# Optimization experiments

Measured on AMD Instinct MI355X. Metric: run time of the kernel, lower is better.

Reference implementation:

```python
import jax, jax.numpy as jnp
import numpy as np

N, D, H2, E = 4096, 1024, 4096, 8  # tokens, input_dim, 2*hidden_dim, num_experts
H = H2 // 2


def setup_inputs() -> dict:
    key = jax.random.key(0)
    k1, k2, k3 = jax.random.split(key, 3)
    x = jax.random.normal(k1, (N, D), dtype=jnp.float32)
    expert_weights = jax.random.normal(k2, (E, D, H2), dtype=jnp.float32) * (1.0 / np.sqrt(D))
    expert_indices = jax.random.randint(k3, (N,), 0, E, dtype=jnp.int32)
    return {"x": x, "expert_weights": expert_weights, "expert_indices": expert_indices}


def reference(x, expert_weights, expert_indices):
    # Grouped GEMM equivalent: each token n is processed by expert e = expert_indices[n]:
    #   h_n = x_n @ W_e            -> [2H]
    #   out_n = silu(h[:H]) * h[H:] (SwiGLU)
    # jit-friendly dense-dispatch: project with all experts, then gather the assigned one.
    h_all = jnp.einsum('nd,edh->neh', x, expert_weights)            # [N, E, 2H]
    h = jnp.take_along_axis(h_all, expert_indices[:, None, None].astype(jnp.int32), axis=1)[:, 0]  # [N, 2H]
    a, b = h[:, :H], h[:, H:]
    return jax.nn.silu(a) * b                                        # [N, H]
```

## Files before the change

kernel.cpp:

```cpp
#include <hip/hip_runtime.h>
#include <hip/hip_bf16.h>

#define N_TOK 4096
#define DIM   1024
#define H2V   4096
#define HV    2048
#define NE    8
#define BM    128
#define BN    64
#define BK    64
#define NTHR  256
#define ROW_TILES (N_TOK / BM)

typedef __attribute__((ext_vector_type(4))) float  f32x4;
typedef __attribute__((ext_vector_type(2))) float  f32x2;
typedef __attribute__((ext_vector_type(8))) short  s16x8;

__device__ __forceinline__ unsigned short f2bf(float f) {
    __hip_bfloat16 h = __float2bfloat16(f);
    union { __hip_bfloat16 h; unsigned short u; } v;
    v.h = h;
    return v.u;
}

__global__ void k_init(int* __restrict__ counts) {
    if (threadIdx.x < NE) counts[threadIdx.x] = 0;
}

__global__ void k_scatter(const int* __restrict__ idx, int* __restrict__ counts,
                          unsigned short* __restrict__ slots) {
    int n = blockIdx.x * blockDim.x + threadIdx.x;
    if (n < N_TOK) {
        int e = idx[n];
        int p = atomicAdd(&counts[e], 1);
        slots[e * N_TOK + p] = (unsigned short)n;
    }
}

__global__ __launch_bounds__(NTHR, 2) void k_gemm(
        const float* __restrict__ X, const float* __restrict__ W,
        const int* __restrict__ counts, const unsigned short* __restrict__ slots,
        float* __restrict__ out) {
    const int ct = blockIdx.x;
    const int e  = blockIdx.y >> 5;
    const int rt = blockIdx.y & 31;
    const int cnt = counts[e];
    const int tbase = rt * BM;
    if (tbase >= cnt) return;
    const unsigned short* ids = slots + e * N_TOK;

    __shared__ unsigned short As[BM * BK];
    __shared__ unsigned short Bs[2 * BN * BK];

    const int t    = threadIdx.x;
    const int lane = t & 63;
    const int wid  = t >> 6;
    const int wm   = wid >> 1;
    const int wn   = wid & 1;
    const int l16  = lane & 15;
    const int g16  = lane >> 4;

    const float* Wb = W + (size_t)e * ((size_t)DIM * H2V);

    const float* a_src[4];
    int a_row[4], a_q0[4];
#pragma unroll
    for (int p = 0; p < 4; ++p) {
        int pp = p * NTHR + t;
        a_row[p] = pp >> 3;
        a_q0[p]  = pp & 7;
        int slot = tbase + a_row[p];
        int tok  = ids[min(slot, cnt - 1)];
        a_src[p] = X + (size_t)tok * DIM + a_q0[p] * 8;
    }
    const float* b_src[2];
    int b_c0[2], b_ko[2];
#pragma unroll
    for (int p = 0; p < 2; ++p) {
        int m2 = p * NTHR + t;
        int cp = m2 & 63;
        int ko = m2 >> 6;
        int c0 = cp * 2;
        int gc = ct * BN + (c0 & 63) + (c0 >> 6) * HV;
        b_src[p] = Wb + (size_t)(ko * 8) * H2V + gc;
        b_c0[p] = c0;
        b_ko[p] = ko;
    }

    f32x4 acc[2][4][2];
    const f32x4 zero = {0.f, 0.f, 0.f, 0.f};
#pragma unroll
    for (int g = 0; g < 2; ++g)
#pragma unroll
        for (int m = 0; m < 4; ++m)
#pragma unroll
            for (int n = 0; n < 2; ++n)
                acc[g][m][n] = zero;

    for (int ks = 0; ks < DIM / BK; ++ks) {
        const int kbase = ks * BK;
        f32x4 av[4][2];
#pragma unroll
        for (int p = 0; p < 4; ++p) {
            const float* s = a_src[p] + kbase;
            av[p][0] = *(const f32x4*)(s);
            av[p][1] = *(const f32x4*)(s + 4);
        }
        f32x2 bv[2][8];
#pragma unroll
        for (int p = 0; p < 2; ++p) {
            const float* s = b_src[p] + (size_t)kbase * H2V;
#pragma unroll
            for (int i = 0; i < 8; ++i)
                bv[p][i] = *(const f32x2*)(s + (size_t)i * H2V);
        }
        __syncthreads();
#pragma unroll
        for (int p = 0; p < 4; ++p) {
            int row = a_row[p], q0 = a_q0[p];
            unsigned short tmp[8];
#pragma unroll
            for (int i = 0; i < 4; ++i) tmp[i]     = f2bf(av[p][0][i]);
#pragma unroll
            for (int i = 0; i < 4; ++i) tmp[4 + i] = f2bf(av[p][1][i]);
            *(s16x8*)((char*)As + row * (BK * 2) + ((q0 ^ (row & 7)) << 4)) =
                *(const s16x8*)tmp;
        }
#pragma unroll
        for (int p = 0; p < 2; ++p) {
            int ko = b_ko[p];
#pragma unroll
            for (int j = 0; j < 2; ++j) {
                int c = b_c0[p] + j;
                unsigned short tmp[8];
#pragma unroll
                for (int i = 0; i < 8; ++i) tmp[i] = f2bf(bv[p][i][j]);
                *(s16x8*)((char*)Bs + c * (BK * 2) + ((ko ^ ((c >> 1) & 7)) << 4)) =
                    *(const s16x8*)tmp;
            }
        }
        __syncthreads();
#pragma unroll
        for (int kk = 0; kk < 2; ++kk) {
            s16x8 af[4], bfr[2][2];
            const int gran = kk * 4 + g16;
#pragma unroll
            for (int m = 0; m < 4; ++m) {
                int row = wm * 64 + m * 16 + l16;
                af[m] = *(const s16x8*)((const char*)As + row * (BK * 2) +
                                        ((gran ^ (row & 7)) << 4));
            }
#pragma unroll
            for (int g = 0; g < 2; ++g)
#pragma unroll
                for (int n = 0; n < 2; ++n) {
                    int c = g * BN + wn * 32 + n * 16 + l16;
                    bfr[g][n] = *(const s16x8*)((const char*)Bs + c * (BK * 2) +
                                                ((gran ^ ((c >> 1) & 7)) << 4));
                }
#pragma unroll
            for (int g = 0; g < 2; ++g)
#pragma unroll
                for (int m = 0; m < 4; ++m)
#pragma unroll
                    for (int n = 0; n < 2; ++n)
                        acc[g][m][n] = __builtin_amdgcn_mfma_f32_16x16x32_bf16(
                            af[m], bfr[g][n], acc[g][m][n], 0, 0, 0);
        }
    }

#pragma unroll
    for (int m = 0; m < 4; ++m) {
#pragma unroll
        for (int r = 0; r < 4; ++r) {
            int rowt = wm * 64 + m * 16 + g16 * 4 + r;
            int slot = tbase + rowt;
            if (slot < cnt) {
                int tok = ids[slot];
#pragma unroll
                for (int n = 0; n < 2; ++n) {
                    int col = ct * BN + wn * 32 + n * 16 + l16;
                    float a = acc[0][m][n][r];
                    float b = acc[1][m][n][r];
                    float sg = a / (1.0f + __expf(-a));
                    out[(size_t)tok * HV + col] = sg * b;
                }
            }
        }
    }
}

extern "C" void kernel_launch(void* const* d_in, const int* in_sizes, int n_in,
                              void* d_out, int out_size, void* d_ws, size_t ws_size,
                              hipStream_t stream) {
    const float* X  = (const float*)d_in[0];
    const float* W  = (const float*)d_in[1];
    const int* idx  = (const int*)d_in[2];
    float* out      = (float*)d_out;

    int* counts = (int*)d_ws;
    unsigned short* slots = (unsigned short*)((char*)d_ws + 64);

    k_init<<<1, 64, 0, stream>>>(counts);
    k_scatter<<<N_TOK / 256, 256, 0, stream>>>(idx, counts, slots);
    dim3 grid(HV / BN, NE * ROW_TILES);
    k_gemm<<<grid, NTHR, 0, stream>>>(X, W, counts, slots, out);
}
```

Before: 104.2 us.

## Pre-gather tokens to bf16 buffer and async-load A tiles into LDS

Adds a prefix-sum kernel and a gather kernel that permute tokens into expert-contiguous order and convert them to bf16 once. The GEMM then loads A tiles with global_load_lds into double-buffered shared memory, prefetching the next step while computing. This removes the repeated fp32 loads and conversions of X across the column tiles. B loads are widened to 16-byte vectors and use a new swizzle. It adds two small launches and a workspace buffer, raises launch_bounds occupancy to 3, and may read past an expert's rows into the next expert's data or past the end of the buffer (these rows are masked at store).

```diff
diff --git a/kernel.cpp b/kernel.cpp
--- a/kernel.cpp
+++ b/kernel.cpp
@@ -10,16 +10,20 @@
 #define BN    64
 #define BK    64
 #define NTHR  256
+#define KSTEPS (DIM / BK)
 #define ROW_TILES (N_TOK / BM)
 
+#define WS_COUNTS 0
+#define WS_BASE   64
+#define WS_SLOTS  128
+#define WS_XPERM  66560
+
 typedef __attribute__((ext_vector_type(4))) float  f32x4;
-typedef __attribute__((ext_vector_type(2))) float  f32x2;
 typedef __attribute__((ext_vector_type(8))) short  s16x8;
 
 __device__ __forceinline__ unsigned short f2bf(float f) {
-    __hip_bfloat16 h = __float2bfloat16(f);
     union { __hip_bfloat16 h; unsigned short u; } v;
-    v.h = h;
+    v.h = __float2bfloat16(f);
     return v.u;
 }
 
@@ -37,19 +41,52 @@
     }
 }
 
-__global__ __launch_bounds__(NTHR, 2) void k_gemm(
-        const float* __restrict__ X, const float* __restrict__ W,
-        const int* __restrict__ counts, const unsigned short* __restrict__ slots,
-        float* __restrict__ out) {
+__global__ void k_base(const int* __restrict__ counts, int* __restrict__ base) {
+    if (threadIdx.x == 0) {
+        int b = 0;
+#pragma unroll
+        for (int e = 0; e < NE; ++e) { base[e] = b; b += counts[e]; }
+        base[NE] = b;
+    }
+}
+
+__global__ void k_gather(const float* __restrict__ X, const int* __restrict__ base,
+                         const unsigned short* __restrict__ slots,
+                         unsigned short* __restrict__ Xp) {
+    const int r    = blockIdx.x * 4 + (threadIdx.x >> 6);
+    const int lane = threadIdx.x & 63;
+    int e = 0;
+#pragma unroll
+    for (int i = 0; i < NE - 1; ++i) if (r >= base[i + 1]) e = i + 1;
+    const int tok = slots[e * N_TOK + (r - base[e])];
+    const float* src = X + (size_t)tok * DIM + lane * 16;
+    unsigned short* dst = Xp + (size_t)r * DIM + lane * 16;
+    f32x4 v0 = *(const f32x4*)(src);
+    f32x4 v1 = *(const f32x4*)(src + 4);
+    f32x4 v2 = *(const f32x4*)(src + 8);
+    f32x4 v3 = *(const f32x4*)(src + 12);
+    unsigned short t0[8], t1[8];
+#pragma unroll
+    for (int i = 0; i < 4; ++i) { t0[i] = f2bf(v0[i]); t0[4 + i] = f2bf(v1[i]); }
+#pragma unroll
+    for (int i = 0; i < 4; ++i) { t1[i] = f2bf(v2[i]); t1[4 + i] = f2bf(v3[i]); }
+    *(s16x8*)(dst)     = *(const s16x8*)t0;
+    *(s16x8*)(dst + 8) = *(const s16x8*)t1;
+}
+
+__global__ __launch_bounds__(NTHR, 3) void k_gemm(
+        const float* __restrict__ W, const int* __restrict__ counts,
+        const int* __restrict__ base, const unsigned short* __restrict__ slots,
+        const unsigned short* __restrict__ Xp, float* __restrict__ out) {
     const int ct = blockIdx.x;
     const int e  = blockIdx.y >> 5;
     const int rt = blockIdx.y & 31;
     const int cnt = counts[e];
     const int tbase = rt * BM;
     if (tbase >= cnt) return;
-    const unsigned short* ids = slots + e * N_TOK;
-
-    __shared__ unsigned short As[BM * BK];
+    const int row_g0 = base[e] + tbase;
+
+    __shared__ unsigned short As[2][BM * BK];
     __shared__ unsigned short Bs[2 * BN * BK];
 
     const int t    = threadIdx.x;
@@ -60,32 +97,18 @@
     const int l16  = lane & 15;
     const int g16  = lane >> 4;
 
-    const float* Wb = W + (size_t)e * ((size_t)DIM * H2V);
-
-    const float* a_src[4];
-    int a_row[4], a_q0[4];
-#pragma unroll
-    for (int p = 0; p < 4; ++p) {
-        int pp = p * NTHR + t;
-        a_row[p] = pp >> 3;
-        a_q0[p]  = pp & 7;
-        int slot = tbase + a_row[p];
-        int tok  = ids[min(slot, cnt - 1)];
-        a_src[p] = X + (size_t)tok * DIM + a_q0[p] * 8;
-    }
-    const float* b_src[2];
-    int b_c0[2], b_ko[2];
-#pragma unroll
-    for (int p = 0; p < 2; ++p) {
-        int m2 = p * NTHR + t;
-        int cp = m2 & 63;
-        int ko = m2 >> 6;
-        int c0 = cp * 2;
-        int gc = ct * BN + (c0 & 63) + (c0 >> 6) * HV;
-        b_src[p] = Wb + (size_t)(ko * 8) * H2V + gc;
-        b_c0[p] = c0;
-        b_ko[p] = ko;
-    }
+    const unsigned short* aptr[4];
+#pragma unroll
+    for (int j = 0; j < 4; ++j) {
+        int i  = wid * 4 + j;
+        int rl = i * 8 + (lane >> 3);
+        int qs = (lane & 7) ^ ((lane >> 3) & 7);
+        aptr[j] = Xp + (size_t)(row_g0 + rl) * DIM + qs * 8;
+    }
+    const int c0 = (t & 31) * 4;
+    const int ko = t >> 5;
+    const int gc = ct * BN + (c0 & 63) + (c0 >> 6) * HV;
+    const float* bptr = W + (size_t)e * DIM * H2V + (size_t)(ko * 8) * H2V + gc;
 
     f32x4 acc[2][4][2];
     const f32x4 zero = {0.f, 0.f, 0.f, 0.f};
@@ -94,69 +117,67 @@
 #pragma unroll
         for (int m = 0; m < 4; ++m)
 #pragma unroll
-            for (int n = 0; n < 2; ++n)
-                acc[g][m][n] = zero;
-
-    for (int ks = 0; ks < DIM / BK; ++ks) {
-        const int kbase = ks * BK;
-        f32x4 av[4][2];
-#pragma unroll
-        for (int p = 0; p < 4; ++p) {
-            const float* s = a_src[p] + kbase;
-            av[p][0] = *(const f32x4*)(s);
-            av[p][1] = *(const f32x4*)(s + 4);
-        }
-        f32x2 bv[2][8];
-#pragma unroll
-        for (int p = 0; p < 2; ++p) {
-            const float* s = b_src[p] + (size_t)kbase * H2V;
-#pragma unroll
-            for (int i = 0; i < 8; ++i)
-                bv[p][i] = *(const f32x2*)(s + (size_t)i * H2V);
-        }
-        __syncthreads();
-#pragma unroll
-        for (int p = 0; p < 4; ++p) {
-            int row = a_row[p], q0 = a_q0[p];
+            for (int n = 0; n < 2; ++n) acc[g][m][n] = zero;
+
+    f32x4 bv[8];
+
+    auto issueA = [&](int ks, int buf) {
+#pragma unroll
+        for (int j = 0; j < 4; ++j) {
+            const unsigned short* g = aptr[j] + ks * BK;
+            unsigned short* l = (unsigned short*)&As[buf][(wid * 4 + j) * 512];
+            __builtin_amdgcn_global_load_lds(
+                (const __attribute__((address_space(1))) unsigned int*)(const void*)g,
+                (__attribute__((address_space(3))) unsigned int*)(void*)l, 16, 0, 0);
+        }
+    };
+    auto loadB = [&](int ks) {
+#pragma unroll
+        for (int i = 0; i < 8; ++i)
+            bv[i] = *(const f32x4*)(bptr + (size_t)(ks * BK + i) * H2V);
+    };
+    auto storeB = [&]() {
+#pragma unroll
+        for (int j = 0; j < 4; ++j) {
+            int c = c0 + j;
+            int key = ((c >> 1) ^ (c >> 4)) & 7;
             unsigned short tmp[8];
 #pragma unroll
-            for (int i = 0; i < 4; ++i) tmp[i]     = f2bf(av[p][0][i]);
-#pragma unroll
-            for (int i = 0; i < 4; ++i) tmp[4 + i] = f2bf(av[p][1][i]);
-            *(s16x8*)((char*)As + row * (BK * 2) + ((q0 ^ (row & 7)) << 4)) =
-                *(const s16x8*)tmp;
-        }
-#pragma unroll
-        for (int p = 0; p < 2; ++p) {
-            int ko = b_ko[p];
-#pragma unroll
-            for (int j = 0; j < 2; ++j) {
-                int c = b_c0[p] + j;
-                unsigned short tmp[8];
-#pragma unroll
-                for (int i = 0; i < 8; ++i) tmp[i] = f2bf(bv[p][i][j]);
-                *(s16x8*)((char*)Bs + c * (BK * 2) + ((ko ^ ((c >> 1) & 7)) << 4)) =
-                    *(const s16x8*)tmp;
-            }
-        }
-        __syncthreads();
+            for (int i = 0; i < 8; ++i) tmp[i] = f2bf(bv[i][j]);
+            *(s16x8*)&Bs[c * 64 + ((ko ^ key) * 8)] = *(const s16x8*)tmp;
+        }
+    };
+
+    issueA(0, 0);
+    loadB(0);
+
+    for (int ks = 0; ks < KSTEPS; ++ks) {
+        const int cur = ks & 1;
+        asm volatile("s_waitcnt vmcnt(0)" ::: "memory");
+        __builtin_amdgcn_s_barrier();
+        storeB();
+        if (ks + 1 < KSTEPS) {
+            issueA(ks + 1, cur ^ 1);
+            loadB(ks + 1);
+        }
+        asm volatile("s_waitcnt lgkmcnt(0)" ::: "memory");
+        __builtin_amdgcn_s_barrier();
 #pragma unroll
         for (int kk = 0; kk < 2; ++kk) {
+            const int gran = kk * 4 + g16;
             s16x8 af[4], bfr[2][2];
-            const int gran = kk * 4 + g16;
 #pragma unroll
             for (int m = 0; m < 4; ++m) {
                 int row = wm * 64 + m * 16 + l16;
-                af[m] = *(const s16x8*)((const char*)As + row * (BK * 2) +
-                                        ((gran ^ (row & 7)) << 4));
+                af[m] = *(const s16x8*)&As[cur][row * 64 + ((gran ^ (row & 7)) * 8)];
             }
 #pragma unroll
             for (int g = 0; g < 2; ++g)
 #pragma unroll
                 for (int n = 0; n < 2; ++n) {
                     int c = g * BN + wn * 32 + n * 16 + l16;
-                    bfr[g][n] = *(const s16x8*)((const char*)Bs + c * (BK * 2) +
-                                                ((gran ^ ((c >> 1) & 7)) << 4));
+                    int key = ((c >> 1) ^ (c >> 4)) & 7;
+                    bfr[g][n] = *(const s16x8*)&Bs[c * 64 + ((gran ^ key) * 8)];
                 }
 #pragma unroll
             for (int g = 0; g < 2; ++g)
@@ -169,6 +190,7 @@
         }
     }
 
+    const unsigned short* ids = slots + e * N_TOK;
 #pragma unroll
     for (int m = 0; m < 4; ++m) {
 #pragma unroll
@@ -198,11 +220,15 @@
     const int* idx  = (const int*)d_in[2];
     float* out      = (float*)d_out;
 
-    int* counts = (int*)d_ws;
-    unsigned short* slots = (unsigned short*)((char*)d_ws + 64);
+    int* counts = (int*)((char*)d_ws + WS_COUNTS);
+    int* base   = (int*)((char*)d_ws + WS_BASE);
+    unsigned short* slots = (unsigned short*)((char*)d_ws + WS_SLOTS);
+    unsigned short* Xp    = (unsigned short*)((char*)d_ws + WS_XPERM);
 
     k_init<<<1, 64, 0, stream>>>(counts);
     k_scatter<<<N_TOK / 256, 256, 0, stream>>>(idx, counts, slots);
+    k_base<<<1, 64, 0, stream>>>(counts, base);
+    k_gather<<<N_TOK / 4, 256, 0, stream>>>(X, base, slots, Xp);
     dim3 grid(HV / BN, NE * ROW_TILES);
-    k_gemm<<<grid, NTHR, 0, stream>>>(X, W, counts, slots, out);
-}
+    k_gemm<<<grid, NTHR, 0, stream>>>(W, counts, base, slots, Xp, out);
+}
```

Measured after the change: 96.59 us. 7.3% less time.
